# Optimization experiments

Hardware: AMD Instinct MI355X
Metric: run time of the kernel (lower is better)

The kernel has to match this reference:

```python
import jax, jax.numpy as jnp
import numpy as np

D = 512        # sinusoidal embedding dimension (BoxTerm/PositionTerm input_dimension)
OUT_DIM = 256  # output_dimension
K = 49         # output_size ** 2


def _denoms(c):
    i = np.arange(1, c, 2).astype(np.float64)  # sin exponents
    j = np.arange(0, c, 2).astype(np.float64)  # cos exponents
    return (jnp.asarray(1000.0 ** (i / c), jnp.float32),
            jnp.asarray(1000.0 ** (j / c), jnp.float32))

_DS, _DC = _denoms(D)


def embed(z):
    # z: [...] -> [..., D] ; cat(sin(z/1000^(i/D)) for odd i, cos(z/1000^(j/D)) for even j)
    zz = z[..., None]
    return jnp.concatenate([jnp.sin(zz / _DS), jnp.cos(zz / _DC)], axis=-1)


def setup_inputs() -> dict:
    key = jax.random.key(0)
    ks = jax.random.split(key, 8)
    B, C, H, W, N = 4, 256, 64, 48, 32
    x = jax.random.normal(ks[0], (B, C, H, W), jnp.float32)
    idx = jax.random.randint(ks[1], (N,), 0, B).astype(jnp.float32)
    coords = jax.random.uniform(ks[2], (N, 4), jnp.float32) * 60.0
    rois = jnp.concatenate([idx[:, None], coords], axis=1)  # [N,5]
    s = 0.02  # param scale to keep softmax logits in a sane range
    V_box = jax.random.normal(ks[3], (D, 4 * D), jnp.float32) * s
    W_box = jax.random.normal(ks[4], (K, OUT_DIM, D), jnp.float32) * s
    W_im = jax.random.normal(ks[5], (OUT_DIM, 2 * D), jnp.float32) * s
    conv_w = jax.random.normal(ks[6], (K, C), jnp.float32) * s
    conv_b = jax.random.normal(ks[7], (K,), jnp.float32) * s
    return {"x": x, "rois": rois, "V_box": V_box, "W_box": W_box,
            "W_im": W_im, "conv_w": conv_w, "conv_b": conv_b}


def reference(x, rois, V_box, W_box, W_im, conv_w, conv_b):
    B, C, H, W = x.shape
    N = rois.shape[0]
    idx = rois[:, 0].astype(jnp.int32)              # batch index per box
    coords = rois[:, 1:]                            # [N,4]
    # BoxTerm: eps [N,4D] -> v = V_box @ eps -> per-k W_box_k @ v
    eps = embed(coords).reshape(N, 4 * D)           # [N,4D]
    v = jnp.einsum('df,nf->nd', V_box, eps)         # [N,D]
    bvec = jnp.einsum('kod,nd->nko', W_box, v)      # [N,K,OUT_DIM]
    # PositionTerm: identical for every image -> compute once
    ex = embed(jnp.arange(H, dtype=jnp.float32))    # [H,D]
    ey = embed(jnp.arange(W, dtype=jnp.float32))    # [W,D]
    pos = jnp.concatenate([jnp.broadcast_to(ex[:, None, :], (H, W, D)),
                           jnp.broadcast_to(ey[None, :, :], (H, W, D))], axis=-1)
    img = jnp.einsum('oe,hwe->hwo', W_im, pos)      # [H,W,OUT_DIM]
    # GeometricTerm: per box, per k: (1,OUT_DIM) @ (H,W,OUT_DIM,1)
    geo = jnp.einsum('nko,hwo->nkhw', bvec, img)    # [N,K,H,W]
    # AppearanceTerm: 1x1 conv
    app = jnp.einsum('bchw,oc->bohw', x, conv_w) + conv_b[None, :, None, None]  # [B,K,H,W]
    # LearnableRoIPool: softmax2d(app + geo_box) over channel dim per box
    logits = app[None, :, :, :, :] + geo[:, None, :, :, :]  # [N,B,K,H,W]
    weights = jax.nn.softmax(logits, axis=2)
    # original emits boxes grouped by image index (stable order within image)
    order = jnp.argsort(idx, stable=True)
    return weights[order]
```

## Files before the change

kernel.cpp:

```cpp
#include <hip/hip_runtime.h>

typedef __attribute__((ext_vector_type(8))) short short8;
typedef __attribute__((ext_vector_type(4))) short short4v;
typedef __attribute__((ext_vector_type(4))) float f32x4;

#define LN1000_OVER_512 0.0134917095f

#define EPS_OFF   0
#define IMGB_OFF  65536
#define V_OFF     79872
#define GX_OFF    96256
#define GY_OFF    196608
#define BVB_OFF   271872
#define APPT_OFF  472576

__device__ __forceinline__ short f2bf(float x) {
  unsigned u = __float_as_uint(x);
  return (short)((u + 0x7FFFu + ((u >> 16) & 1u)) >> 16);
}
__device__ __forceinline__ short4v f2bf4(float4 v) {
  short4v r; r.x = f2bf(v.x); r.y = f2bf(v.y); r.z = f2bf(v.z); r.w = f2bf(v.w);
  return r;
}

__global__ __launch_bounds__(256) void k1(const float* __restrict__ rois,
                                          const float* __restrict__ W_im,
                                          const float* __restrict__ x,
                                          const float* __restrict__ conv_w,
                                          const float* __restrict__ conv_b,
                                          float* __restrict__ ws) {
  __shared__ __align__(16) short sh[96 * 264];
  int bid = blockIdx.x, tid = threadIdx.x;
  short* imgb = (short*)(ws + IMGB_OFF);
  if (bid < 112) {
    float* el = (float*)sh;
    bool isx = bid < 64;
    int pos = isx ? bid : bid - 64;
    float z = (float)pos;
    for (int e = tid; e < 512; e += 256) {
      float inv = (e < 256) ? __expf(-LN1000_OVER_512 * (float)(2*e+1))
                            : __expf(-LN1000_OVER_512 * (float)(2*(e-256)));
      el[e] = (e < 256) ? __sinf(z * inv) : __cosf(z * inv);
    }
    __syncthreads();
    const float* wrow = W_im + tid * 1024 + (isx ? 0 : 512);
    float acc = 0.f;
    #pragma unroll 4
    for (int d = 0; d < 512; d += 4) {
      float4 wv = *(const float4*)(wrow + d);
      acc += wv.x*el[d] + wv.y*el[d+1] + wv.z*el[d+2] + wv.w*el[d+3];
    }
    imgb[bid * 256 + tid] = f2bf(acc);
  } else if (bid < 120) {
    int id0 = (bid - 112) * 256 + tid;
    for (int r = 0; r < 32; ++r) {
      int id = id0 + r * 2048;
      int n = id >> 11, f = id & 2047;
      int c = f >> 9, e = f & 511;
      float z = rois[n*5 + 1 + c];
      float inv = (e < 256) ? __expf(-LN1000_OVER_512 * (float)(2*e+1))
                            : __expf(-LN1000_OVER_512 * (float)(2*(e-256)));
      ws[EPS_OFF + id] = (e < 256) ? __sinf(z*inv) : __cosf(z*inv);
    }
  } else if (bid == 120) {
    #pragma unroll
    for (int i = 0; i < 64; ++i) ws[V_OFF + tid + i*256] = 0.f;
  } else {
    short* Al = sh;
    short* Bl = sh + 32*264;
    int t = bid - 121;
    int b = t / 96, pt = t % 96;
    int p0 = pt * 32;
    const float* xb = x + (size_t)b * 786432;
    #pragma unroll
    for (int j = 0; j < 8; ++j) {
      int fid = tid + j*256;
      int c = fid >> 3, pj = fid & 7;
      float4 v = *(const float4*)(xb + c*3072 + p0 + pj*4);
      Al[(pj*4+0)*264 + c] = f2bf(v.x);
      Al[(pj*4+1)*264 + c] = f2bf(v.y);
      Al[(pj*4+2)*264 + c] = f2bf(v.z);
      Al[(pj*4+3)*264 + c] = f2bf(v.w);
    }
    #pragma unroll
    for (int j = 0; j < 16; ++j) {
      int fid = tid + j*256;
      int k = fid >> 6, c4 = fid & 63;
      short4v s4 = {0,0,0,0};
      if (k < 49) s4 = f2bf4(*(const float4*)(conv_w + k*256 + c4*4));
      *(short4v*)(Bl + k*264 + c4*4) = s4;
    }
    __syncthreads();
    int w = tid >> 6, lane = tid & 63;
    int q = lane >> 4, m = lane & 15;
    int n0 = w * 16;
    f32x4 acc0 = {0.f,0.f,0.f,0.f}, acc1 = {0.f,0.f,0.f,0.f};
    const short* ap = Al + m*264 + q*8;
    const short* bp = Bl + (n0+m)*264 + q*8;
    #pragma unroll
    for (int kk = 0; kk < 8; ++kk) {
      short8 b8 = *(const short8*)(bp + kk*32);
      short8 a0 = *(const short8*)(ap + kk*32);
      short8 a1 = *(const short8*)(ap + 16*264 + kk*32);
      acc0 = __builtin_amdgcn_mfma_f32_16x16x32_bf16(a0, b8, acc0, 0,0,0);
      acc1 = __builtin_amdgcn_mfma_f32_16x16x32_bf16(a1, b8, acc1, 0,0,0);
    }
    int k = n0 + m;
    if (k < 49) {
      float bias = conv_b[k];
      float* apt = ws + APPT_OFF + (size_t)b * 159744;
      #pragma unroll
      for (int r = 0; r < 4; ++r) {
        int p = p0 + q*4 + r;
        apt[(size_t)p*52 + k] = acc0[r] + bias;
        apt[(size_t)(p+16)*52 + k] = acc1[r] + bias;
      }
    }
  }
}

__global__ __launch_bounds__(256) void k2(const float* __restrict__ V_box,
                                          float* __restrict__ ws) {
  __shared__ __align__(16) short Al[32*264];
  __shared__ __align__(16) short Bl[32*264];
  int tid = threadIdx.x;
  int ntb = blockIdx.x & 15, ks = blockIdx.x >> 4;
  int k0 = ks * 256, d0 = ntb * 32;
  #pragma unroll
  for (int j = 0; j < 8; ++j) {
    int fid = tid + j*256;
    int n = fid >> 6, k4 = fid & 63;
    float4 v = *(const float4*)(ws + EPS_OFF + n*2048 + k0 + k4*4);
    *(short4v*)(Al + n*264 + k4*4) = f2bf4(v);
  }
  #pragma unroll
  for (int j = 0; j < 8; ++j) {
    int fid = tid + j*256;
    int dd = fid >> 6, k4 = fid & 63;
    float4 v = *(const float4*)(V_box + (size_t)(d0+dd)*2048 + k0 + k4*4);
    *(short4v*)(Bl + dd*264 + k4*4) = f2bf4(v);
  }
  __syncthreads();
  int w = tid >> 6, lane = tid & 63;
  int q = lane >> 4, m = lane & 15;
  int m0 = (w & 1)*16, n0 = (w >> 1)*16;
  f32x4 acc = {0.f,0.f,0.f,0.f};
  const short* ap = Al + (m0+m)*264 + q*8;
  const short* bp = Bl + (n0+m)*264 + q*8;
  #pragma unroll
  for (int kk = 0; kk < 8; ++kk) {
    short8 a = *(const short8*)(ap + kk*32);
    short8 b = *(const short8*)(bp + kk*32);
    acc = __builtin_amdgcn_mfma_f32_16x16x32_bf16(a, b, acc, 0, 0, 0);
  }
  #pragma unroll
  for (int r = 0; r < 4; ++r) {
    int row = m0 + q*4 + r;
    int col = d0 + n0 + m;
    unsafeAtomicAdd(&ws[V_OFF + row*512 + col], acc[r]);
  }
}

__global__ __launch_bounds__(256) void k3(const float* __restrict__ W_box,
                                          float* __restrict__ ws) {
  __shared__ __align__(16) short Av[32*520];
  __shared__ __align__(16) short Bl[32*520];
  int tid = threadIdx.x;
  int j0 = blockIdx.x * 32;
  #pragma unroll
  for (int j = 0; j < 16; ++j) {
    int fid = tid + j*256;
    int n = fid >> 7, d4 = fid & 127;
    float4 v = *(const float4*)(ws + V_OFF + n*512 + d4*4);
    *(short4v*)(Av + n*520 + d4*4) = f2bf4(v);
  }
  #pragma unroll
  for (int j = 0; j < 16; ++j) {
    int fid = tid + j*256;
    int rr = fid >> 7, d4 = fid & 127;
    float4 v = *(const float4*)(W_box + (size_t)(j0+rr)*512 + d4*4);
    *(short4v*)(Bl + rr*520 + d4*4) = f2bf4(v);
  }
  __syncthreads();
  int w = tid >> 6, lane = tid & 63;
  int q = lane >> 4, m = lane & 15;
  int m0 = (w & 1)*16, n0 = (w >> 1)*16;
  f32x4 acc = {0.f,0.f,0.f,0.f};
  const short* ap = Av + (m0+m)*520 + q*8;
  const short* bp = Bl + (n0+m)*520 + q*8;
  #pragma unroll
  for (int kk = 0; kk < 16; ++kk) {
    short8 a = *(const short8*)(ap + kk*32);
    short8 b = *(const short8*)(bp + kk*32);
    acc = __builtin_amdgcn_mfma_f32_16x16x32_bf16(a, b, acc, 0, 0, 0);
  }
  short* bvb = (short*)(ws + BVB_OFF);
  #pragma unroll
  for (int r = 0; r < 4; ++r) {
    int row = m0 + q*4 + r;
    int col = j0 + n0 + m;
    bvb[(size_t)row*12544 + col] = f2bf(acc[r]);
  }
}

__global__ __launch_bounds__(256) void k4(float* __restrict__ ws) {
  __shared__ __align__(16) short Al[32*264];
  int tid = threadIdx.x;
  int half = blockIdx.x & 1, rb = blockIdx.x >> 1;
  int r0 = rb * 32;
  const short* bvb = (const short*)(ws + BVB_OFF);
  #pragma unroll
  for (int j = 0; j < 4; ++j) {
    int fid = tid + j*256;
    int rr = fid >> 5, o8 = fid & 31;
    *(short8*)(Al + rr*264 + o8*8) = *(const short8*)(bvb + (size_t)(r0+rr)*256 + o8*8);
  }
  __syncthreads();
  int w = tid >> 6, lane = tid & 63;
  int q = lane >> 4, m = lane & 15;
  int nct = half ? 3 : 4;
  if (w < nct) {
    const short* imgb = (const short*)(ws + IMGB_OFF) + (half ? 64*256 : 0);
    int ct = w;
    f32x4 acc0 = {0.f,0.f,0.f,0.f}, acc1 = {0.f,0.f,0.f,0.f};
    const short* ap0 = Al + m*264 + q*8;
    const short* ap1 = Al + (16+m)*264 + q*8;
    const short* bp  = imgb + (ct*16+m)*256 + q*8;
    #pragma unroll
    for (int kk = 0; kk < 8; ++kk) {
      short8 b8 = *(const short8*)(bp + kk*32);
      short8 a0 = *(const short8*)(ap0 + kk*32);
      short8 a1 = *(const short8*)(ap1 + kk*32);
      acc0 = __builtin_amdgcn_mfma_f32_16x16x32_bf16(a0, b8, acc0, 0,0,0);
      acc1 = __builtin_amdgcn_mfma_f32_16x16x32_bf16(a1, b8, acc1, 0,0,0);
    }
    float* outp = ws + (half ? GY_OFF : GX_OFF);
    int stride = half ? 48 : 64;
    int col = ct*16 + m;
    #pragma unroll
    for (int r = 0; r < 4; ++r) {
      outp[(r0 + q*4 + r)*stride + col]      = acc0[r];
      outp[(r0 + 16 + q*4 + r)*stride + col] = acc1[r];
    }
  }
}

__global__ __launch_bounds__(256) void k5(const float* __restrict__ rois,
                                          const float* __restrict__ ws,
                                          float* __restrict__ out) {
  __shared__ float gxl[3136];
  __shared__ float gyl[2352];
  __shared__ int rank_sh;
  int tid = threadIdx.x, bid = blockIdx.x;
  int n = bid / 12, tile = bid % 12;
  #pragma unroll
  for (int j = 0; j < 4; ++j) {
    int id = tid + j*256;
    if (id < 784) *(float4*)(gxl + id*4) = *(const float4*)(ws + GX_OFF + n*3136 + id*4);
  }
  #pragma unroll
  for (int j = 0; j < 3; ++j) {
    int id = tid + j*256;
    if (id < 588) *(float4*)(gyl + id*4) = *(const float4*)(ws + GY_OFF + n*2352 + id*4);
  }
  if (tid == 0) {
    float my = rois[n*5];
    int r = 0;
    for (int mm = 0; mm < 32; ++mm) {
      float vm = rois[mm*5];
      if (vm < my || (vm == my && mm < n)) ++r;
    }
    rank_sh = r;
  }
  __syncthreads();
  int pix = tile*256 + tid;
  int h = pix / 48, wv = pix - h*48;
  int r = rank_sh;
  for (int b = 0; b < 4; ++b) {
    const float* ap = ws + APPT_OFF + (size_t)(b*3072 + pix)*52;
    float lg[49];
    #pragma unroll
    for (int qq = 0; qq < 12; ++qq) {
      float4 t = *(const float4*)(ap + qq*4);
      lg[qq*4+0] = t.x; lg[qq*4+1] = t.y; lg[qq*4+2] = t.z; lg[qq*4+3] = t.w;
    }
    lg[48] = ap[48];
    #pragma unroll
    for (int k = 0; k < 49; ++k)
      lg[k] += gxl[k*64 + h] + gyl[k*48 + wv];
    float mx = lg[0];
    #pragma unroll
    for (int k = 1; k < 49; ++k) mx = fmaxf(mx, lg[k]);
    float s = 0.f;
    #pragma unroll
    for (int k = 0; k < 49; ++k) { float e = __expf(lg[k]-mx); lg[k] = e; s += e; }
    float inv = 1.f / s;
    float* op = out + (size_t)(r*4 + b)*150528 + pix;
    #pragma unroll
    for (int k = 0; k < 49; ++k)
      op[(size_t)k*3072] = lg[k]*inv;
  }
}

extern "C" void kernel_launch(void* const* d_in, const int* in_sizes, int n_in,
                              void* d_out, int out_size, void* d_ws, size_t ws_size,
                              hipStream_t stream) {
  const float* x      = (const float*)d_in[0];
  const float* rois   = (const float*)d_in[1];
  const float* V_box  = (const float*)d_in[2];
  const float* W_box  = (const float*)d_in[3];
  const float* W_im   = (const float*)d_in[4];
  const float* conv_w = (const float*)d_in[5];
  const float* conv_b = (const float*)d_in[6];
  float* ws  = (float*)d_ws;
  float* out = (float*)d_out;

  hipLaunchKernelGGL(k1, dim3(505), dim3(256), 0, stream, rois, W_im, x, conv_w, conv_b, ws);
  hipLaunchKernelGGL(k2, dim3(128), dim3(256), 0, stream, V_box, ws);
  hipLaunchKernelGGL(k3, dim3(392), dim3(256), 0, stream, W_box, ws);
  hipLaunchKernelGGL(k4, dim3(98),  dim3(256), 0, stream, ws);
  hipLaunchKernelGGL(k5, dim3(384), dim3(256), 0, stream, rois, ws, out);
}
```

Before: 151.6 us.

## Fuse embedding into GEMMs, drop atomics, fold geo GEMM into softmax kernel

Cuts the pipeline from five kernels to three. The box and position sinusoidal embeddings are now computed directly into LDS inside MFMA GEMM blocks; the position GEMM moves from a scalar dot product to MFMA. The V split-K reduction writes four partial buffers that the next kernel sums, replacing the zero-init pass and the atomics. The geometric GEMM (bvec x img) is computed per box inside the softmax kernel, so the old k4 launch and its gx/gy round trip through global memory go away. The cost is that the geo GEMM is recomputed in each of the 12 tiles per box, and the V sum now uses float partials in a different order.

```diff
diff --git a/kernel.cpp b/kernel.cpp
--- a/kernel.cpp
+++ b/kernel.cpp
@@ -6,13 +6,10 @@
 
 #define LN1000_OVER_512 0.0134917095f
 
-#define EPS_OFF   0
-#define IMGB_OFF  65536
-#define V_OFF     79872
-#define GX_OFF    96256
-#define GY_OFF    196608
-#define BVB_OFF   271872
-#define APPT_OFF  472576
+#define IMGB_OFF  0
+#define PARTV_OFF 14336
+#define BVB_OFF   79872
+#define APPT_OFF  280576
 
 __device__ __forceinline__ short f2bf(float x) {
   unsigned u = __float_as_uint(x);
@@ -25,85 +22,130 @@
 
 __global__ __launch_bounds__(256) void k1(const float* __restrict__ rois,
                                           const float* __restrict__ W_im,
+                                          const float* __restrict__ V_box,
                                           const float* __restrict__ x,
                                           const float* __restrict__ conv_w,
                                           const float* __restrict__ conv_b,
                                           float* __restrict__ ws) {
   __shared__ __align__(16) short sh[96 * 264];
   int bid = blockIdx.x, tid = threadIdx.x;
-  short* imgb = (short*)(ws + IMGB_OFF);
-  if (bid < 112) {
-    float* el = (float*)sh;
-    bool isx = bid < 64;
-    int pos = isx ? bid : bid - 64;
-    float z = (float)pos;
-    for (int e = tid; e < 512; e += 256) {
-      float inv = (e < 256) ? __expf(-LN1000_OVER_512 * (float)(2*e+1))
-                            : __expf(-LN1000_OVER_512 * (float)(2*(e-256)));
-      el[e] = (e < 256) ? __sinf(z * inv) : __cosf(z * inv);
-    }
-    __syncthreads();
-    const float* wrow = W_im + tid * 1024 + (isx ? 0 : 512);
-    float acc = 0.f;
-    #pragma unroll 4
-    for (int d = 0; d < 512; d += 4) {
-      float4 wv = *(const float4*)(wrow + d);
-      acc += wv.x*el[d] + wv.y*el[d+1] + wv.z*el[d+2] + wv.w*el[d+3];
-    }
-    imgb[bid * 256 + tid] = f2bf(acc);
-  } else if (bid < 120) {
-    int id0 = (bid - 112) * 256 + tid;
-    for (int r = 0; r < 32; ++r) {
-      int id = id0 + r * 2048;
-      int n = id >> 11, f = id & 2047;
-      int c = f >> 9, e = f & 511;
-      float z = rois[n*5 + 1 + c];
-      float inv = (e < 256) ? __expf(-LN1000_OVER_512 * (float)(2*e+1))
-                            : __expf(-LN1000_OVER_512 * (float)(2*(e-256)));
-      ws[EPS_OFF + id] = (e < 256) ? __sinf(z*inv) : __cosf(z*inv);
-    }
-  } else if (bid == 120) {
-    #pragma unroll
-    for (int i = 0; i < 64; ++i) ws[V_OFF + tid + i*256] = 0.f;
+  int w = tid >> 6, lane = tid & 63;
+  int q = lane >> 4, m = lane & 15;
+
+  if (bid < 96) {
+    short* Al = sh;
+    short* Bl = sh + 32 * 264;
+    float inv_s = __expf(-LN1000_OVER_512 * (float)(2 * tid + 1));
+    float inv_c = __expf(-LN1000_OVER_512 * (float)(2 * tid));
+    f32x4 acc = {0.f, 0.f, 0.f, 0.f};
+    int m0 = (w & 1) * 16, n0 = (w >> 1) * 16;
+
+    if (bid < 64) {
+      int ntb = bid & 15, ks = bid >> 4;
+      int d0 = ntb * 32;
+      for (int c = 0; c < 2; ++c) {
+        int k0 = ks * 512 + c * 256;
+        for (int j = 0; j < 32; ++j) {
+          float z = rois[j * 5 + 1 + ks];
+          float val = c ? __cosf(z * inv_c) : __sinf(z * inv_s);
+          Al[j * 264 + tid] = f2bf(val);
+        }
+        #pragma unroll
+        for (int jj = 0; jj < 8; ++jj) {
+          int fid = tid + jj * 256;
+          int dd = fid >> 6, k4 = fid & 63;
+          float4 v = *(const float4*)(V_box + (size_t)(d0 + dd) * 2048 + k0 + k4 * 4);
+          *(short4v*)(Bl + dd * 264 + k4 * 4) = f2bf4(v);
+        }
+        __syncthreads();
+        const short* ap = Al + (m0 + m) * 264 + q * 8;
+        const short* bp = Bl + (n0 + m) * 264 + q * 8;
+        #pragma unroll
+        for (int kk = 0; kk < 8; ++kk) {
+          short8 a = *(const short8*)(ap + kk * 32);
+          short8 b = *(const short8*)(bp + kk * 32);
+          acc = __builtin_amdgcn_mfma_f32_16x16x32_bf16(a, b, acc, 0, 0, 0);
+        }
+        __syncthreads();
+      }
+      #pragma unroll
+      for (int r = 0; r < 4; ++r)
+        ws[PARTV_OFF + ks * 16384 + (m0 + q * 4 + r) * 512 + d0 + n0 + m] = acc[r];
+    } else {
+      int t = bid - 64;
+      int mt = t >> 3, nt = t & 7;
+      int rm0 = mt * 32, o0 = nt * 32;
+      int khalf = mt >> 1;
+      int posbase = rm0 - khalf * 64;
+      for (int c = 0; c < 2; ++c) {
+        int k0 = khalf * 512 + c * 256;
+        for (int j = 0; j < 32; ++j) {
+          float z = (float)(posbase + j);
+          float val = c ? __cosf(z * inv_c) : __sinf(z * inv_s);
+          Al[j * 264 + tid] = f2bf(val);
+        }
+        #pragma unroll
+        for (int jj = 0; jj < 8; ++jj) {
+          int fid = tid + jj * 256;
+          int dd = fid >> 6, k4 = fid & 63;
+          float4 v = *(const float4*)(W_im + (size_t)(o0 + dd) * 1024 + k0 + k4 * 4);
+          *(short4v*)(Bl + dd * 264 + k4 * 4) = f2bf4(v);
+        }
+        __syncthreads();
+        const short* ap = Al + (m0 + m) * 264 + q * 8;
+        const short* bp = Bl + (n0 + m) * 264 + q * 8;
+        #pragma unroll
+        for (int kk = 0; kk < 8; ++kk) {
+          short8 a = *(const short8*)(ap + kk * 32);
+          short8 b = *(const short8*)(bp + kk * 32);
+          acc = __builtin_amdgcn_mfma_f32_16x16x32_bf16(a, b, acc, 0, 0, 0);
+        }
+        __syncthreads();
+      }
+      short* imgb = (short*)(ws + IMGB_OFF);
+      #pragma unroll
+      for (int r = 0; r < 4; ++r) {
+        int row = rm0 + m0 + q * 4 + r;
+        if (row < 112) imgb[row * 256 + o0 + n0 + m] = f2bf(acc[r]);
+      }
+    }
   } else {
     short* Al = sh;
-    short* Bl = sh + 32*264;
-    int t = bid - 121;
+    short* Bl = sh + 32 * 264;
+    int t = bid - 96;
     int b = t / 96, pt = t % 96;
     int p0 = pt * 32;
     const float* xb = x + (size_t)b * 786432;
     #pragma unroll
     for (int j = 0; j < 8; ++j) {
-      int fid = tid + j*256;
+      int fid = tid + j * 256;
       int c = fid >> 3, pj = fid & 7;
-      float4 v = *(const float4*)(xb + c*3072 + p0 + pj*4);
-      Al[(pj*4+0)*264 + c] = f2bf(v.x);
-      Al[(pj*4+1)*264 + c] = f2bf(v.y);
-      Al[(pj*4+2)*264 + c] = f2bf(v.z);
-      Al[(pj*4+3)*264 + c] = f2bf(v.w);
+      float4 v = *(const float4*)(xb + c * 3072 + p0 + pj * 4);
+      Al[(pj * 4 + 0) * 264 + c] = f2bf(v.x);
+      Al[(pj * 4 + 1) * 264 + c] = f2bf(v.y);
+      Al[(pj * 4 + 2) * 264 + c] = f2bf(v.z);
+      Al[(pj * 4 + 3) * 264 + c] = f2bf(v.w);
     }
     #pragma unroll
     for (int j = 0; j < 16; ++j) {
-      int fid = tid + j*256;
+      int fid = tid + j * 256;
       int k = fid >> 6, c4 = fid & 63;
-      short4v s4 = {0,0,0,0};
-      if (k < 49) s4 = f2bf4(*(const float4*)(conv_w + k*256 + c4*4));
-      *(short4v*)(Bl + k*264 + c4*4) = s4;
+      short4v s4 = {0, 0, 0, 0};
+      if (k < 49) s4 = f2bf4(*(const float4*)(conv_w + k * 256 + c4 * 4));
+      *(short4v*)(Bl + k * 264 + c4 * 4) = s4;
     }
     __syncthreads();
-    int w = tid >> 6, lane = tid & 63;
-    int q = lane >> 4, m = lane & 15;
     int n0 = w * 16;
-    f32x4 acc0 = {0.f,0.f,0.f,0.f}, acc1 = {0.f,0.f,0.f,0.f};
-    const short* ap = Al + m*264 + q*8;
-    const short* bp = Bl + (n0+m)*264 + q*8;
+    f32x4 acc0 = {0.f, 0.f, 0.f, 0.f}, acc1 = {0.f, 0.f, 0.f, 0.f};
+    const short* ap = Al + m * 264 + q * 8;
+    const short* bp = Bl + (n0 + m) * 264 + q * 8;
     #pragma unroll
     for (int kk = 0; kk < 8; ++kk) {
-      short8 b8 = *(const short8*)(bp + kk*32);
-      short8 a0 = *(const short8*)(ap + kk*32);
-      short8 a1 = *(const short8*)(ap + 16*264 + kk*32);
-      acc0 = __builtin_amdgcn_mfma_f32_16x16x32_bf16(a0, b8, acc0, 0,0,0);
-      acc1 = __builtin_amdgcn_mfma_f32_16x16x32_bf16(a1, b8, acc1, 0,0,0);
+      short8 b8 = *(const short8*)(bp + kk * 32);
+      short8 a0 = *(const short8*)(ap + kk * 32);
+      short8 a1 = *(const short8*)(ap + 16 * 264 + kk * 32);
+      acc0 = __builtin_amdgcn_mfma_f32_16x16x32_bf16(a0, b8, acc0, 0, 0, 0);
+      acc1 = __builtin_amdgcn_mfma_f32_16x16x32_bf16(a1, b8, acc1, 0, 0, 0);
     }
     int k = n0 + m;
     if (k < 49) {
@@ -111,194 +153,133 @@
       float* apt = ws + APPT_OFF + (size_t)b * 159744;
       #pragma unroll
       for (int r = 0; r < 4; ++r) {
-        int p = p0 + q*4 + r;
-        apt[(size_t)p*52 + k] = acc0[r] + bias;
-        apt[(size_t)(p+16)*52 + k] = acc1[r] + bias;
+        int p = p0 + q * 4 + r;
+        apt[(size_t)p * 52 + k] = acc0[r] + bias;
+        apt[(size_t)(p + 16) * 52 + k] = acc1[r] + bias;
       }
     }
   }
 }
 
-__global__ __launch_bounds__(256) void k2(const float* __restrict__ V_box,
+__global__ __launch_bounds__(256) void k2(const float* __restrict__ W_box,
                                           float* __restrict__ ws) {
-  __shared__ __align__(16) short Al[32*264];
-  __shared__ __align__(16) short Bl[32*264];
-  int tid = threadIdx.x;
-  int ntb = blockIdx.x & 15, ks = blockIdx.x >> 4;
-  int k0 = ks * 256, d0 = ntb * 32;
-  #pragma unroll
-  for (int j = 0; j < 8; ++j) {
-    int fid = tid + j*256;
-    int n = fid >> 6, k4 = fid & 63;
-    float4 v = *(const float4*)(ws + EPS_OFF + n*2048 + k0 + k4*4);
-    *(short4v*)(Al + n*264 + k4*4) = f2bf4(v);
-  }
-  #pragma unroll
-  for (int j = 0; j < 8; ++j) {
-    int fid = tid + j*256;
-    int dd = fid >> 6, k4 = fid & 63;
-    float4 v = *(const float4*)(V_box + (size_t)(d0+dd)*2048 + k0 + k4*4);
-    *(short4v*)(Bl + dd*264 + k4*4) = f2bf4(v);
-  }
-  __syncthreads();
-  int w = tid >> 6, lane = tid & 63;
-  int q = lane >> 4, m = lane & 15;
-  int m0 = (w & 1)*16, n0 = (w >> 1)*16;
-  f32x4 acc = {0.f,0.f,0.f,0.f};
-  const short* ap = Al + (m0+m)*264 + q*8;
-  const short* bp = Bl + (n0+m)*264 + q*8;
-  #pragma unroll
-  for (int kk = 0; kk < 8; ++kk) {
-    short8 a = *(const short8*)(ap + kk*32);
-    short8 b = *(const short8*)(bp + kk*32);
-    acc = __builtin_amdgcn_mfma_f32_16x16x32_bf16(a, b, acc, 0, 0, 0);
-  }
-  #pragma unroll
-  for (int r = 0; r < 4; ++r) {
-    int row = m0 + q*4 + r;
-    int col = d0 + n0 + m;
-    unsafeAtomicAdd(&ws[V_OFF + row*512 + col], acc[r]);
-  }
-}
-
-__global__ __launch_bounds__(256) void k3(const float* __restrict__ W_box,
-                                          float* __restrict__ ws) {
-  __shared__ __align__(16) short Av[32*520];
-  __shared__ __align__(16) short Bl[32*520];
+  __shared__ __align__(16) short Av[32 * 520];
+  __shared__ __align__(16) short Bl[32 * 520];
   int tid = threadIdx.x;
   int j0 = blockIdx.x * 32;
   #pragma unroll
   for (int j = 0; j < 16; ++j) {
-    int fid = tid + j*256;
+    int fid = tid + j * 256;
     int n = fid >> 7, d4 = fid & 127;
-    float4 v = *(const float4*)(ws + V_OFF + n*512 + d4*4);
-    *(short4v*)(Av + n*520 + d4*4) = f2bf4(v);
+    const float* p = ws + PARTV_OFF + n * 512 + d4 * 4;
+    float4 v0 = *(const float4*)(p);
+    float4 v1 = *(const float4*)(p + 16384);
+    float4 v2 = *(const float4*)(p + 32768);
+    float4 v3 = *(const float4*)(p + 49152);
+    float4 s; s.x = v0.x + v1.x + v2.x + v3.x; s.y = v0.y + v1.y + v2.y + v3.y;
+    s.z = v0.z + v1.z + v2.z + v3.z; s.w = v0.w + v1.w + v2.w + v3.w;
+    *(short4v*)(Av + n * 520 + d4 * 4) = f2bf4(s);
   }
   #pragma unroll
   for (int j = 0; j < 16; ++j) {
-    int fid = tid + j*256;
+    int fid = tid + j * 256;
     int rr = fid >> 7, d4 = fid & 127;
-    float4 v = *(const float4*)(W_box + (size_t)(j0+rr)*512 + d4*4);
-    *(short4v*)(Bl + rr*520 + d4*4) = f2bf4(v);
+    float4 v = *(const float4*)(W_box + (size_t)(j0 + rr) * 512 + d4 * 4);
+    *(short4v*)(Bl + rr * 520 + d4 * 4) = f2bf4(v);
   }
   __syncthreads();
   int w = tid >> 6, lane = tid & 63;
   int q = lane >> 4, m = lane & 15;
-  int m0 = (w & 1)*16, n0 = (w >> 1)*16;
-  f32x4 acc = {0.f,0.f,0.f,0.f};
-  const short* ap = Av + (m0+m)*520 + q*8;
-  const short* bp = Bl + (n0+m)*520 + q*8;
+  int m0 = (w & 1) * 16, n0 = (w >> 1) * 16;
+  f32x4 acc = {0.f, 0.f, 0.f, 0.f};
+  const short* ap = Av + (m0 + m) * 520 + q * 8;
+  const short* bp = Bl + (n0 + m) * 520 + q * 8;
   #pragma unroll
   for (int kk = 0; kk < 16; ++kk) {
-    short8 a = *(const short8*)(ap + kk*32);
-    short8 b = *(const short8*)(bp + kk*32);
+    short8 a = *(const short8*)(ap + kk * 32);
+    short8 b = *(const short8*)(bp + kk * 32);
     acc = __builtin_amdgcn_mfma_f32_16x16x32_bf16(a, b, acc, 0, 0, 0);
   }
   short* bvb = (short*)(ws + BVB_OFF);
   #pragma unroll
   for (int r = 0; r < 4; ++r) {
-    int row = m0 + q*4 + r;
+    int row = m0 + q * 4 + r;
     int col = j0 + n0 + m;
-    bvb[(size_t)row*12544 + col] = f2bf(acc[r]);
-  }
-}
-
-__global__ __launch_bounds__(256) void k4(float* __restrict__ ws) {
-  __shared__ __align__(16) short Al[32*264];
-  int tid = threadIdx.x;
-  int half = blockIdx.x & 1, rb = blockIdx.x >> 1;
-  int r0 = rb * 32;
-  const short* bvb = (const short*)(ws + BVB_OFF);
-  #pragma unroll
-  for (int j = 0; j < 4; ++j) {
-    int fid = tid + j*256;
-    int rr = fid >> 5, o8 = fid & 31;
-    *(short8*)(Al + rr*264 + o8*8) = *(const short8*)(bvb + (size_t)(r0+rr)*256 + o8*8);
-  }
-  __syncthreads();
-  int w = tid >> 6, lane = tid & 63;
-  int q = lane >> 4, m = lane & 15;
-  int nct = half ? 3 : 4;
-  if (w < nct) {
-    const short* imgb = (const short*)(ws + IMGB_OFF) + (half ? 64*256 : 0);
-    int ct = w;
-    f32x4 acc0 = {0.f,0.f,0.f,0.f}, acc1 = {0.f,0.f,0.f,0.f};
-    const short* ap0 = Al + m*264 + q*8;
-    const short* ap1 = Al + (16+m)*264 + q*8;
-    const short* bp  = imgb + (ct*16+m)*256 + q*8;
-    #pragma unroll
-    for (int kk = 0; kk < 8; ++kk) {
-      short8 b8 = *(const short8*)(bp + kk*32);
-      short8 a0 = *(const short8*)(ap0 + kk*32);
-      short8 a1 = *(const short8*)(ap1 + kk*32);
-      acc0 = __builtin_amdgcn_mfma_f32_16x16x32_bf16(a0, b8, acc0, 0,0,0);
-      acc1 = __builtin_amdgcn_mfma_f32_16x16x32_bf16(a1, b8, acc1, 0,0,0);
-    }
-    float* outp = ws + (half ? GY_OFF : GX_OFF);
-    int stride = half ? 48 : 64;
-    int col = ct*16 + m;
-    #pragma unroll
-    for (int r = 0; r < 4; ++r) {
-      outp[(r0 + q*4 + r)*stride + col]      = acc0[r];
-      outp[(r0 + 16 + q*4 + r)*stride + col] = acc1[r];
-    }
-  }
-}
-
-__global__ __launch_bounds__(256) void k5(const float* __restrict__ rois,
+    bvb[(size_t)row * 12544 + col] = f2bf(acc[r]);
+  }
+}
+
+__global__ __launch_bounds__(256) void k3(const float* __restrict__ rois,
                                           const float* __restrict__ ws,
                                           float* __restrict__ out) {
-  __shared__ float gxl[3136];
-  __shared__ float gyl[2352];
+  __shared__ float gxl[64 * 64];
+  __shared__ float gyl[64 * 48];
   __shared__ int rank_sh;
   int tid = threadIdx.x, bid = blockIdx.x;
   int n = bid / 12, tile = bid % 12;
-  #pragma unroll
-  for (int j = 0; j < 4; ++j) {
-    int id = tid + j*256;
-    if (id < 784) *(float4*)(gxl + id*4) = *(const float4*)(ws + GX_OFF + n*3136 + id*4);
-  }
-  #pragma unroll
-  for (int j = 0; j < 3; ++j) {
-    int id = tid + j*256;
-    if (id < 588) *(float4*)(gyl + id*4) = *(const float4*)(ws + GY_OFF + n*2352 + id*4);
-  }
+  int w = tid >> 6, lane = tid & 63;
+  int q = lane >> 4, m = lane & 15;
+  const short* bvb  = (const short*)(ws + BVB_OFF);
+  const short* imgb = (const short*)(ws + IMGB_OFF);
+
   if (tid == 0) {
-    float my = rois[n*5];
+    float my = rois[n * 5];
     int r = 0;
     for (int mm = 0; mm < 32; ++mm) {
-      float vm = rois[mm*5];
+      float vm = rois[mm * 5];
       if (vm < my || (vm == my && mm < n)) ++r;
     }
     rank_sh = r;
   }
+
+  for (int t = w; t < 28; t += 4) {
+    int kt, rB; bool isy = t >= 16;
+    if (!isy) { kt = t >> 2; rB = (t & 3) * 16; }
+    else { int tt = t - 16; kt = tt / 3; rB = 64 + (tt % 3) * 16; }
+    f32x4 acc = {0.f, 0.f, 0.f, 0.f};
+    const short* ap = bvb + ((size_t)n * 49 + kt * 16 + m) * 256 + q * 8;
+    const short* bp = imgb + (rB + m) * 256 + q * 8;
+    #pragma unroll
+    for (int s = 0; s < 8; ++s) {
+      short8 a = *(const short8*)(ap + s * 32);
+      short8 b = *(const short8*)(bp + s * 32);
+      acc = __builtin_amdgcn_mfma_f32_16x16x32_bf16(a, b, acc, 0, 0, 0);
+    }
+    #pragma unroll
+    for (int r = 0; r < 4; ++r) {
+      int kk = kt * 16 + q * 4 + r;
+      if (!isy) gxl[kk * 64 + rB + m] = acc[r];
+      else      gyl[kk * 48 + (rB - 64) + m] = acc[r];
+    }
+  }
   __syncthreads();
-  int pix = tile*256 + tid;
-  int h = pix / 48, wv = pix - h*48;
+
+  int pix = tile * 256 + tid;
+  int h = pix / 48, wv = pix - h * 48;
   int r = rank_sh;
   for (int b = 0; b < 4; ++b) {
-    const float* ap = ws + APPT_OFF + (size_t)(b*3072 + pix)*52;
+    const float* ap = ws + APPT_OFF + (size_t)(b * 3072 + pix) * 52;
     float lg[49];
     #pragma unroll
     for (int qq = 0; qq < 12; ++qq) {
-      float4 t = *(const float4*)(ap + qq*4);
-      lg[qq*4+0] = t.x; lg[qq*4+1] = t.y; lg[qq*4+2] = t.z; lg[qq*4+3] = t.w;
+      float4 tv = *(const float4*)(ap + qq * 4);
+      lg[qq * 4 + 0] = tv.x; lg[qq * 4 + 1] = tv.y; lg[qq * 4 + 2] = tv.z; lg[qq * 4 + 3] = tv.w;
     }
     lg[48] = ap[48];
     #pragma unroll
     for (int k = 0; k < 49; ++k)
-      lg[k] += gxl[k*64 + h] + gyl[k*48 + wv];
+      lg[k] += gxl[k * 64 + h] + gyl[k * 48 + wv];
     float mx = lg[0];
     #pragma unroll
     for (int k = 1; k < 49; ++k) mx = fmaxf(mx, lg[k]);
     float s = 0.f;
     #pragma unroll
-    for (int k = 0; k < 49; ++k) { float e = __expf(lg[k]-mx); lg[k] = e; s += e; }
+    for (int k = 0; k < 49; ++k) { float e = __expf(lg[k] - mx); lg[k] = e; s += e; }
     float inv = 1.f / s;
-    float* op = out + (size_t)(r*4 + b)*150528 + pix;
+    float* op = out + (size_t)(r * 4 + b) * 150528 + pix;
     #pragma unroll
     for (int k = 0; k < 49; ++k)
-      op[(size_t)k*3072] = lg[k]*inv;
+      op[(size_t)k * 3072] = lg[k] * inv;
   }
 }
 
@@ -315,9 +296,7 @@
   float* ws  = (float*)d_ws;
   float* out = (float*)d_out;
 
-  hipLaunchKernelGGL(k1, dim3(505), dim3(256), 0, stream, rois, W_im, x, conv_w, conv_b, ws);
-  hipLaunchKernelGGL(k2, dim3(128), dim3(256), 0, stream, V_box, ws);
-  hipLaunchKernelGGL(k3, dim3(392), dim3(256), 0, stream, W_box, ws);
-  hipLaunchKernelGGL(k4, dim3(98),  dim3(256), 0, stream, ws);
-  hipLaunchKernelGGL(k5, dim3(384), dim3(256), 0, stream, rois, ws, out);
-}
+  hipLaunchKernelGGL(k1, dim3(480), dim3(256), 0, stream, rois, W_im, V_box, x, conv_w, conv_b, ws);
+  hipLaunchKernelGGL(k2, dim3(392), dim3(256), 0, stream, W_box, ws);
+  hipLaunchKernelGGL(k3, dim3(384), dim3(256), 0, stream, rois, ws, out);
+}
```

Measured after the change: 156.7 us. +3.4%, slower.
